# Optimization experiments

Hardware: AMD Instinct MI355X
Metric: run time of the kernel (lower is better)

The kernel has to match this reference:

```python
import jax, jax.numpy as jnp
import numpy as np

HEADS = 4
DIM_HEAD = 32
SCALE = DIM_HEAD ** -0.5


def setup_inputs() -> dict:
    key = jax.random.key(0)
    k1, k2, k3 = jax.random.split(key, 3)
    dim = 128
    hidden = HEADS * DIM_HEAD  # 128
    x = jax.random.normal(k1, (4, dim, 64, 64), dtype=jnp.float32)
    w_qkv = jax.random.normal(k2, (3 * hidden, dim), dtype=jnp.float32) * (dim ** -0.5)
    w_out = jax.random.normal(k3, (dim, hidden), dtype=jnp.float32) * (hidden ** -0.5)
    b_out = jnp.zeros((dim,), dtype=jnp.float32)
    return {"x": x, "w_qkv": w_qkv, "w_out": w_out, "b_out": b_out}


def reference(x, w_qkv, w_out, b_out):
    b, c, h, w = x.shape
    n = h * w
    # 1x1 conv == channel matmul per pixel
    qkv = jnp.einsum('oc,bchw->bohw', w_qkv, x)  # [b, 3*hidden, h, w]
    q, k, v = jnp.split(qkv, 3, axis=1)
    # b (heads d) x y -> b heads d (x y)
    def to_heads(t):
        return t.reshape(b, HEADS, DIM_HEAD, n)
    q = to_heads(q) * SCALE
    k = to_heads(k)
    v = to_heads(v)
    sim = jnp.einsum('bhdi,bhdj->bhij', q, k)          # [b, heads, n, n]
    attn = jax.nn.softmax(sim, axis=-1)
    out = jnp.einsum('bhij,bhdj->bhid', attn, v)        # [b, heads, n, d]
    # b h (x y) d -> b (h d) x y
    out = out.transpose(0, 1, 3, 2).reshape(b, HEADS * DIM_HEAD, h, w)
    out = jnp.einsum('oc,bchw->bohw', w_out, out) + b_out[None, :, None, None]
    return out
```

## Files before the change

### kernel.cpp

```cpp
#include <hip/hip_runtime.h>
#include <math.h>

#define NHEAD 4
#define DHEAD 32
#define NPIX  4096
#define CIN   128

typedef __bf16 bf16_t;
typedef __bf16 bf16x8 __attribute__((ext_vector_type(8)));
typedef __bf16 bf16x4 __attribute__((ext_vector_type(4)));
typedef float  f32x4  __attribute__((ext_vector_type(4)));

constexpr float QSCALE = 0.17677669529663687f * 1.4426950408889634f;

__global__ void __launch_bounds__(256) prep_swz(
    const float* __restrict__ wqkv, const float* __restrict__ wout,
    ushort* __restrict__ wq_s, ushort* __restrict__ wo_s) {
  const int gid = blockIdx.x * 256 + threadIdx.x;
  const int lane = gid & 63, n = lane & 15, quad = (lane >> 4) & 3;
  if (gid < 6144) {
    const int ot = gid >> 8, k = (gid >> 6) & 3;
    const float sc = (ot < 8) ? QSCALE : 1.f;
    const float* src = wqkv + (size_t)(ot * 16 + n) * CIN + k * 32 + quad * 8;
    bf16x8 o;
#pragma unroll
    for (int e = 0; e < 8; ++e) o[e] = (bf16_t)(src[e] * sc);
    *(bf16x8*)(wq_s + (size_t)gid * 8) = o;
  } else {
    const int oid = gid - 6144;
    const int ot = oid >> 8, k = (oid >> 6) & 3;
    const float* src = wout + (size_t)(ot * 16 + n) * CIN + k * 32 + quad * 8;
    bf16x8 o;
#pragma unroll
    for (int e = 0; e < 8; ++e) o[e] = (bf16_t)src[e];
    *(bf16x8*)(wo_s + (size_t)oid * 8) = o;
  }
}

__global__ void __launch_bounds__(256) qkv_mfma(
    const float* __restrict__ x, const ushort* __restrict__ wq_s,
    ushort* __restrict__ qb, ushort* __restrict__ kb, ushort* __restrict__ vT) {
  __shared__ ushort Xls[32 * 136];
  const int blk = blockIdx.x, tid = threadIdx.x;
  const int half = blockIdx.y;
  const int wave = tid >> 6, lane = tid & 63;
  const int n = lane & 15, quad = lane >> 4;
  const int bb = blk >> 7;
  const int p0 = (blk & 127) * 32;

  {
    const int pc = tid & 7, c0 = (tid >> 3) * 4;
    const float* xp = x + ((size_t)bb * CIN + c0) * NPIX + p0 + pc * 4;
    float4 r0 = *(const float4*)xp;
    float4 r1 = *(const float4*)(xp + NPIX);
    float4 r2 = *(const float4*)(xp + 2 * NPIX);
    float4 r3 = *(const float4*)(xp + 3 * NPIX);
    bf16x4 w0 = {(bf16_t)r0.x, (bf16_t)r1.x, (bf16_t)r2.x, (bf16_t)r3.x};
    bf16x4 w1 = {(bf16_t)r0.y, (bf16_t)r1.y, (bf16_t)r2.y, (bf16_t)r3.y};
    bf16x4 w2 = {(bf16_t)r0.z, (bf16_t)r1.z, (bf16_t)r2.z, (bf16_t)r3.z};
    bf16x4 w3 = {(bf16_t)r0.w, (bf16_t)r1.w, (bf16_t)r2.w, (bf16_t)r3.w};
    *(bf16x4*)&Xls[(pc * 4 + 0) * 136 + c0] = w0;
    *(bf16x4*)&Xls[(pc * 4 + 1) * 136 + c0] = w1;
    *(bf16x4*)&Xls[(pc * 4 + 2) * 136 + c0] = w2;
    *(bf16x4*)&Xls[(pc * 4 + 3) * 136 + c0] = w3;
  }
  __syncthreads();

  bf16x8 xf[2][4];
#pragma unroll
  for (int nt = 0; nt < 2; ++nt)
#pragma unroll
    for (int k = 0; k < 4; ++k)
      xf[nt][k] = *(const bf16x8*)&Xls[(nt * 16 + n) * 136 + k * 32 + quad * 8];

#pragma unroll
  for (int mt = 0; mt < 3; ++mt) {
    const int ot = half * 12 + wave * 3 + mt;
    const int type = ot >> 3;
    const int wt = ot & 7, head = wt >> 1, d0 = (wt & 1) * 16;
    const int bh = bb * NHEAD + head;
    bf16x8 wf4[4];
#pragma unroll
    for (int k = 0; k < 4; ++k)
      wf4[k] = *(const bf16x8*)(wq_s + (size_t)((ot * 4 + k) * 64 + lane) * 8);
    f32x4 acc[2] = {{0.f, 0.f, 0.f, 0.f}, {0.f, 0.f, 0.f, 0.f}};
    if (type < 2) {
#pragma unroll
      for (int k = 0; k < 4; ++k)
#pragma unroll
        for (int nt = 0; nt < 2; ++nt)
          acc[nt] = __builtin_amdgcn_mfma_f32_16x16x32_bf16(wf4[k], xf[nt][k], acc[nt], 0, 0, 0);
      ushort* dst = (type == 0) ? qb : kb;
#pragma unroll
      for (int nt = 0; nt < 2; ++nt) {
        bf16x4 o = {(bf16_t)acc[nt][0], (bf16_t)acc[nt][1],
                    (bf16_t)acc[nt][2], (bf16_t)acc[nt][3]};
        *(bf16x4*)(dst + ((size_t)bh * NPIX + p0 + nt * 16 + n) * DHEAD + d0 + quad * 4) = o;
      }
    } else {
#pragma unroll
      for (int k = 0; k < 4; ++k)
#pragma unroll
        for (int nt = 0; nt < 2; ++nt)
          acc[nt] = __builtin_amdgcn_mfma_f32_16x16x32_bf16(xf[nt][k], wf4[k], acc[nt], 0, 0, 0);
#pragma unroll
      for (int nt = 0; nt < 2; ++nt) {
        bf16x4 o = {(bf16_t)acc[nt][0], (bf16_t)acc[nt][1],
                    (bf16_t)acc[nt][2], (bf16_t)acc[nt][3]};
        *(bf16x4*)(vT + ((size_t)bh * DHEAD + d0 + n) * NPIX + p0 + nt * 16 + quad * 4) = o;
      }
    }
  }
}

__device__ __forceinline__ void ft_load(const ushort* kb0, const ushort* vb0,
                                        int t, bf16x8* kf, bf16x8* vf) {
#pragma unroll
  for (int p = 0; p < 2; ++p) {
#pragma unroll
    for (int s = 0; s < 2; ++s)
      kf[p * 2 + s] = *(const bf16x8*)(kb0 + (size_t)(t * 64 + p * 32 + s * 4) * DHEAD);
#pragma unroll
    for (int dp = 0; dp < 2; ++dp)
      vf[p * 2 + dp] = *(const bf16x8*)(vb0 + (size_t)dp * 16 * NPIX + t * 64 + p * 32);
  }
}

__device__ __forceinline__ void ft_compute(const bf16x8* qf, const bf16x8* kf,
                                           const bf16x8* vf, const bf16x8 ones,
                                           f32x4 O[8][2], f32x4* Ol) {
  const f32x4 zero = {0.f, 0.f, 0.f, 0.f};
  __builtin_amdgcn_s_setprio(1);
#pragma unroll
  for (int p = 0; p < 2; ++p) {
#pragma unroll
    for (int rp = 0; rp < 8; ++rp) {
      f32x4 sa = __builtin_amdgcn_mfma_f32_16x16x32_bf16(kf[p * 2 + 0], qf[rp], zero, 0, 0, 0);
      f32x4 sb = __builtin_amdgcn_mfma_f32_16x16x32_bf16(kf[p * 2 + 1], qf[rp], zero, 0, 0, 0);
      bf16x8 pf;
#pragma unroll
      for (int r = 0; r < 4; ++r) {
        pf[r]     = (bf16_t)__builtin_amdgcn_exp2f(sa[r]);
        pf[r + 4] = (bf16_t)__builtin_amdgcn_exp2f(sb[r]);
      }
      O[rp][0] = __builtin_amdgcn_mfma_f32_16x16x32_bf16(pf, vf[p * 2 + 0], O[rp][0], 0, 0, 0);
      O[rp][1] = __builtin_amdgcn_mfma_f32_16x16x32_bf16(pf, vf[p * 2 + 1], O[rp][1], 0, 0, 0);
      Ol[rp]   = __builtin_amdgcn_mfma_f32_16x16x32_bf16(pf, ones, Ol[rp], 0, 0, 0);
    }
  }
  __builtin_amdgcn_s_setprio(0);
}

__global__ void __launch_bounds__(256, 2) flash_mfma(
    const ushort* __restrict__ qb, const ushort* __restrict__ kbuf,
    const ushort* __restrict__ vTb, float* __restrict__ part) {
  const int tid = threadIdx.x, wave = tid >> 6, lane = tid & 63;
  const int n = lane & 15, quad = lane >> 4;

  const int id = blockIdx.x;
  const int g  = (id & 7) | ((id >> 6) << 3);
  const int qbk = (id >> 3) & 7;
  const int bh = g >> 2;
  const int js = g & 3;
  const int qrel = qbk * 512 + wave * 128;

  const ushort* kg = kbuf + (size_t)bh * NPIX * DHEAD;
  const ushort* vg = vTb + (size_t)bh * DHEAD * NPIX;

  bf16x8 qf[8];
#pragma unroll
  for (int rp = 0; rp < 8; ++rp)
    qf[rp] = *(const bf16x8*)(qb +
        ((size_t)bh * NPIX + qrel + rp * 16 + n) * DHEAD + quad * 8);

  f32x4 O[8][2], Ol[8];
#pragma unroll
  for (int rp = 0; rp < 8; ++rp) {
    O[rp][0] = (f32x4){0.f, 0.f, 0.f, 0.f};
    O[rp][1] = (f32x4){0.f, 0.f, 0.f, 0.f};
    Ol[rp]   = (f32x4){0.f, 0.f, 0.f, 0.f};
  }
  const bf16_t one = (bf16_t)1.0f;
  const bf16x8 ones = {one, one, one, one, one, one, one, one};

  const int pk = ((n >> 2) << 3) | (n & 3);
  const ushort* kb0 = kg + (size_t)(js * 1024 + pk) * DHEAD + quad * 8;
  const ushort* vb0 = vg + (size_t)n * NPIX + js * 1024 + quad * 8;

  bf16x8 kA[4], vA[4], kB[4], vB[4];
  ft_load(kb0, vb0, 0, kA, vA);
#pragma unroll 1
  for (int t = 0; t < 16; t += 2) {
    ft_load(kb0, vb0, t + 1, kB, vB);
    ft_compute(qf, kA, vA, ones, O, Ol);
    if (t + 2 < 16) ft_load(kb0, vb0, t + 2, kA, vA);
    ft_compute(qf, kB, vB, ones, O, Ol);
  }

  float* pb = part + ((size_t)js * 65536 + (size_t)bh * NPIX + qrel) * 36;
#pragma unroll
  for (int rp = 0; rp < 8; ++rp)
#pragma unroll
    for (int r = 0; r < 4; ++r) {
      const int q = rp * 16 + quad * 4 + r;
      pb[(size_t)q * 36 + n]      = O[rp][0][r];
      pb[(size_t)q * 36 + 16 + n] = O[rp][1][r];
      if (n == 0) pb[(size_t)q * 36 + 32] = Ol[rp][r];
    }
}

__global__ void __launch_bounds__(256) out_fused(
    const float* __restrict__ part, const ushort* __restrict__ wo_s,
    const float* __restrict__ bias, float* __restrict__ out) {
  __shared__ ushort AOls[16 * 136];
  const int blk = blockIdx.x, tid = threadIdx.x;
  const int wave = tid >> 6, lane = tid & 63;
  const int n = lane & 15, quad = lane >> 4;
  const int bb = blk >> 8;
  const int p0 = (blk & 255) * 16;
  const int oc0 = wave * 32;

  bf16x8 wf[2][4];
#pragma unroll
  for (int mt = 0; mt < 2; ++mt)
#pragma unroll
    for (int k = 0; k < 4; ++k)
      wf[mt][k] = *(const bf16x8*)(wo_s + (size_t)(((wave * 2 + mt) * 4 + k) * 64 + lane) * 8);

  {
    const int px = tid >> 4, c16 = tid & 15;
    const int h = c16 >> 2, doff = (c16 & 3) * 8;
    const size_t rowbase = (size_t)(bb * NHEAD + h) * NPIX + p0 + px;
    float s[8];
#pragma unroll
    for (int e = 0; e < 8; ++e) s[e] = 0.f;
    float l = 0.f;
#pragma unroll
    for (int js = 0; js < 4; ++js) {
      const float* pp = part + ((size_t)js * 65536 + rowbase) * 36;
      f32x4 a0 = *(const f32x4*)(pp + doff);
      f32x4 a1 = *(const f32x4*)(pp + doff + 4);
#pragma unroll
      for (int e = 0; e < 4; ++e) {
        s[e]     += a0[e];
        s[4 + e] += a1[e];
      }
      l += pp[32];
    }
    const float inv = 1.f / l;
    bf16x8 o0;
#pragma unroll
    for (int e = 0; e < 8; ++e) o0[e] = (bf16_t)(s[e] * inv);
    *(bf16x8*)&AOls[px * 136 + c16 * 8] = o0;
  }
  __syncthreads();

  bf16x8 bfr[4];
#pragma unroll
  for (int k = 0; k < 4; ++k)
    bfr[k] = *(const bf16x8*)&AOls[n * 136 + k * 32 + quad * 8];

  f32x4 acc[2];
#pragma unroll
  for (int mt = 0; mt < 2; ++mt) acc[mt] = (f32x4){0.f, 0.f, 0.f, 0.f};
#pragma unroll
  for (int k = 0; k < 4; ++k)
#pragma unroll
    for (int mt = 0; mt < 2; ++mt)
      acc[mt] = __builtin_amdgcn_mfma_f32_16x16x32_bf16(
          wf[mt][k], bfr[k], acc[mt], 0, 0, 0);

#pragma unroll
  for (int mt = 0; mt < 2; ++mt) {
    const int oc = oc0 + mt * 16 + quad * 4;
#pragma unroll
    for (int r = 0; r < 4; ++r)
      out[((size_t)bb * CIN + oc + r) * NPIX + p0 + n] =
          acc[mt][r] + bias[oc + r];
  }
}

extern "C" void kernel_launch(void* const* d_in, const int* in_sizes, int n_in,
                              void* d_out, int out_size, void* d_ws, size_t ws_size,
                              hipStream_t stream) {
  const float* x     = (const float*)d_in[0];
  const float* w_qkv = (const float*)d_in[1];
  const float* w_out = (const float*)d_in[2];
  const float* b_out = (const float*)d_in[3];
  float* out = (float*)d_out;

  char* base = (char*)d_ws;
  ushort* qb   = (ushort*)base;
  ushort* kb   = (ushort*)(base + (size_t)4 * 1024 * 1024);
  ushort* vT   = (ushort*)(base + (size_t)8 * 1024 * 1024);
  ushort* wq_s = (ushort*)(base + (size_t)12 * 1024 * 1024);
  ushort* wo_s = (ushort*)(base + (size_t)12 * 1024 * 1024 + 256 * 1024);
  float*  part = (float*)(base + (size_t)13 * 1024 * 1024);

  prep_swz<<<dim3(32), 256, 0, stream>>>(w_qkv, w_out, wq_s, wo_s);
  qkv_mfma<<<dim3(512, 2), 256, 0, stream>>>(x, wq_s, qb, kb, vT);
  flash_mfma<<<dim3(512), 256, 0, stream>>>(qb, kb, vT, part);
  out_fused<<<dim3(1024), 256, 0, stream>>>(part, wo_s, b_out, out);
}
```

Measured before the change: 125.6 us.

## Halve query rows per wave for higher occupancy and fold weight prep into consumers

The flash attention kernel now gives each wave 64 query rows instead of 128. This halves its register footprint, lets the launch bound request 4 blocks per CU, and doubles the grid to 1024 blocks. Separately, the weight-swizzle prep kernel is removed: the QKV and output-projection kernels now read fp32 weights directly and convert them to bf16 in registers, saving one launch. The trade-off is that each K/V tile is reused across fewer query rows, so K/V load traffic per unit of compute rises, and every block redoes the weight conversion.

Result: slower. 229.2 us (+82.6%).

```diff
diff --git a/kernel.cpp b/kernel.cpp
--- a/kernel.cpp
+++ b/kernel.cpp
@@ -5,6 +5,7 @@
 #define DHEAD 32
 #define NPIX  4096
 #define CIN   128
+#define RP    4
 
 typedef __bf16 bf16_t;
 typedef __bf16 bf16x8 __attribute__((ext_vector_type(8)));
@@ -13,32 +14,8 @@
 
 constexpr float QSCALE = 0.17677669529663687f * 1.4426950408889634f;
 
-__global__ void __launch_bounds__(256) prep_swz(
-    const float* __restrict__ wqkv, const float* __restrict__ wout,
-    ushort* __restrict__ wq_s, ushort* __restrict__ wo_s) {
-  const int gid = blockIdx.x * 256 + threadIdx.x;
-  const int lane = gid & 63, n = lane & 15, quad = (lane >> 4) & 3;
-  if (gid < 6144) {
-    const int ot = gid >> 8, k = (gid >> 6) & 3;
-    const float sc = (ot < 8) ? QSCALE : 1.f;
-    const float* src = wqkv + (size_t)(ot * 16 + n) * CIN + k * 32 + quad * 8;
-    bf16x8 o;
-#pragma unroll
-    for (int e = 0; e < 8; ++e) o[e] = (bf16_t)(src[e] * sc);
-    *(bf16x8*)(wq_s + (size_t)gid * 8) = o;
-  } else {
-    const int oid = gid - 6144;
-    const int ot = oid >> 8, k = (oid >> 6) & 3;
-    const float* src = wout + (size_t)(ot * 16 + n) * CIN + k * 32 + quad * 8;
-    bf16x8 o;
-#pragma unroll
-    for (int e = 0; e < 8; ++e) o[e] = (bf16_t)src[e];
-    *(bf16x8*)(wo_s + (size_t)oid * 8) = o;
-  }
-}
-
 __global__ void __launch_bounds__(256) qkv_mfma(
-    const float* __restrict__ x, const ushort* __restrict__ wq_s,
+    const float* __restrict__ x, const float* __restrict__ wqkv,
     ushort* __restrict__ qb, ushort* __restrict__ kb, ushort* __restrict__ vT) {
   __shared__ ushort Xls[32 * 136];
   const int blk = blockIdx.x, tid = threadIdx.x;
@@ -79,10 +56,18 @@
     const int type = ot >> 3;
     const int wt = ot & 7, head = wt >> 1, d0 = (wt & 1) * 16;
     const int bh = bb * NHEAD + head;
+    const float sc = (type == 0) ? QSCALE : 1.f;
     bf16x8 wf4[4];
 #pragma unroll
-    for (int k = 0; k < 4; ++k)
-      wf4[k] = *(const bf16x8*)(wq_s + (size_t)((ot * 4 + k) * 64 + lane) * 8);
+    for (int k = 0; k < 4; ++k) {
+      const float* ws = wqkv + (size_t)(ot * 16 + n) * CIN + k * 32 + quad * 8;
+      float4 a = *(const float4*)ws;
+      float4 b = *(const float4*)(ws + 4);
+      wf4[k] = (bf16x8){(bf16_t)(a.x * sc), (bf16_t)(a.y * sc),
+                        (bf16_t)(a.z * sc), (bf16_t)(a.w * sc),
+                        (bf16_t)(b.x * sc), (bf16_t)(b.y * sc),
+                        (bf16_t)(b.z * sc), (bf16_t)(b.w * sc)};
+    }
     f32x4 acc[2] = {{0.f, 0.f, 0.f, 0.f}, {0.f, 0.f, 0.f, 0.f}};
     if (type < 2) {
 #pragma unroll
@@ -128,13 +113,13 @@
 
 __device__ __forceinline__ void ft_compute(const bf16x8* qf, const bf16x8* kf,
                                            const bf16x8* vf, const bf16x8 ones,
-                                           f32x4 O[8][2], f32x4* Ol) {
+                                           f32x4 O[RP][2], f32x4* Ol) {
   const f32x4 zero = {0.f, 0.f, 0.f, 0.f};
   __builtin_amdgcn_s_setprio(1);
 #pragma unroll
   for (int p = 0; p < 2; ++p) {
 #pragma unroll
-    for (int rp = 0; rp < 8; ++rp) {
+    for (int rp = 0; rp < RP; ++rp) {
       f32x4 sa = __builtin_amdgcn_mfma_f32_16x16x32_bf16(kf[p * 2 + 0], qf[rp], zero, 0, 0, 0);
       f32x4 sb = __builtin_amdgcn_mfma_f32_16x16x32_bf16(kf[p * 2 + 1], qf[rp], zero, 0, 0, 0);
       bf16x8 pf;
@@ -151,31 +136,31 @@
   __builtin_amdgcn_s_setprio(0);
 }
 
-__global__ void __launch_bounds__(256, 2) flash_mfma(
+__global__ void __launch_bounds__(256, 4) flash_mfma(
     const ushort* __restrict__ qb, const ushort* __restrict__ kbuf,
     const ushort* __restrict__ vTb, float* __restrict__ part) {
   const int tid = threadIdx.x, wave = tid >> 6, lane = tid & 63;
   const int n = lane & 15, quad = lane >> 4;
 
   const int id = blockIdx.x;
-  const int g  = (id & 7) | ((id >> 6) << 3);
-  const int qbk = (id >> 3) & 7;
+  const int g  = (id & 7) | ((id >> 7) << 3);
+  const int qbk = (id >> 3) & 15;
   const int bh = g >> 2;
   const int js = g & 3;
-  const int qrel = qbk * 512 + wave * 128;
+  const int qrel = qbk * 256 + wave * 64;
 
   const ushort* kg = kbuf + (size_t)bh * NPIX * DHEAD;
   const ushort* vg = vTb + (size_t)bh * DHEAD * NPIX;
 
-  bf16x8 qf[8];
-#pragma unroll
-  for (int rp = 0; rp < 8; ++rp)
+  bf16x8 qf[RP];
+#pragma unroll
+  for (int rp = 0; rp < RP; ++rp)
     qf[rp] = *(const bf16x8*)(qb +
         ((size_t)bh * NPIX + qrel + rp * 16 + n) * DHEAD + quad * 8);
 
-  f32x4 O[8][2], Ol[8];
-#pragma unroll
-  for (int rp = 0; rp < 8; ++rp) {
+  f32x4 O[RP][2], Ol[RP];
+#pragma unroll
+  for (int rp = 0; rp < RP; ++rp) {
     O[rp][0] = (f32x4){0.f, 0.f, 0.f, 0.f};
     O[rp][1] = (f32x4){0.f, 0.f, 0.f, 0.f};
     Ol[rp]   = (f32x4){0.f, 0.f, 0.f, 0.f};
@@ -199,7 +184,7 @@
 
   float* pb = part + ((size_t)js * 65536 + (size_t)bh * NPIX + qrel) * 36;
 #pragma unroll
-  for (int rp = 0; rp < 8; ++rp)
+  for (int rp = 0; rp < RP; ++rp)
 #pragma unroll
     for (int r = 0; r < 4; ++r) {
       const int q = rp * 16 + quad * 4 + r;
@@ -210,7 +195,7 @@
 }
 
 __global__ void __launch_bounds__(256) out_fused(
-    const float* __restrict__ part, const ushort* __restrict__ wo_s,
+    const float* __restrict__ part, const float* __restrict__ wout,
     const float* __restrict__ bias, float* __restrict__ out) {
   __shared__ ushort AOls[16 * 136];
   const int blk = blockIdx.x, tid = threadIdx.x;
@@ -224,8 +209,13 @@
 #pragma unroll
   for (int mt = 0; mt < 2; ++mt)
 #pragma unroll
-    for (int k = 0; k < 4; ++k)
-      wf[mt][k] = *(const bf16x8*)(wo_s + (size_t)(((wave * 2 + mt) * 4 + k) * 64 + lane) * 8);
+    for (int k = 0; k < 4; ++k) {
+      const float* ws = wout + (size_t)((wave * 2 + mt) * 16 + n) * CIN + k * 32 + quad * 8;
+      float4 a = *(const float4*)ws;
+      float4 b = *(const float4*)(ws + 4);
+      wf[mt][k] = (bf16x8){(bf16_t)a.x, (bf16_t)a.y, (bf16_t)a.z, (bf16_t)a.w,
+                           (bf16_t)b.x, (bf16_t)b.y, (bf16_t)b.z, (bf16_t)b.w};
+    }
 
   {
     const int px = tid >> 4, c16 = tid & 15;
@@ -293,12 +283,9 @@
   ushort* qb   = (ushort*)base;
   ushort* kb   = (ushort*)(base + (size_t)4 * 1024 * 1024);
   ushort* vT   = (ushort*)(base + (size_t)8 * 1024 * 1024);
-  ushort* wq_s = (ushort*)(base + (size_t)12 * 1024 * 1024);
-  ushort* wo_s = (ushort*)(base + (size_t)12 * 1024 * 1024 + 256 * 1024);
-  float*  part = (float*)(base + (size_t)13 * 1024 * 1024);
-
-  prep_swz<<<dim3(32), 256, 0, stream>>>(w_qkv, w_out, wq_s, wo_s);
-  qkv_mfma<<<dim3(512, 2), 256, 0, stream>>>(x, wq_s, qb, kb, vT);
-  flash_mfma<<<dim3(512), 256, 0, stream>>>(qb, kb, vT, part);
-  out_fused<<<dim3(1024), 256, 0, stream>>>(part, wo_s, b_out, out);
-}
+  float*  part = (float*)(base + (size_t)12 * 1024 * 1024);
+
+  qkv_mfma<<<dim3(512, 2), 256, 0, stream>>>(x, w_qkv, qb, kb, vT);
+  flash_mfma<<<dim3(1024), 256, 0, stream>>>(qb, kb, vT, part);
+  out_fused<<<dim3(1024), 256, 0, stream>>>(part, w_out, b_out, out);
+}
```
